# Performance work log

Hardware: AMD Instinct MI355X
Metric: run time of the kernel (lower is better)

The kernel has to match this reference:

```python
import jax, jax.numpy as jnp
import numpy as np

D_MODEL = 128; N_HEADS = 8; N_LEVELS = 1; N_POINTS = 8
MAX_RES = 10.0
B, H_SP, W_SP = 8, 64, 64


def setup_inputs() -> dict:
    key = jax.random.key(0)
    ks = jax.random.split(key, 8)
    s = 0.02
    f32 = jnp.float32
    return {
        "nbr_fea": jax.random.normal(ks[0], (B, D_MODEL, H_SP, W_SP), f32),
        "ext_fea": jax.random.normal(ks[1], (B, D_MODEL, H_SP, W_SP), f32),
        "W_val": jax.random.normal(ks[2], (D_MODEL, D_MODEL), f32) * s,
        "b_val": jnp.zeros((D_MODEL,), f32),
        "W_off": jax.random.normal(ks[3], (D_MODEL, N_HEADS * N_LEVELS * N_POINTS * 2), f32) * s,
        "b_off": jax.random.normal(ks[4], (N_HEADS * N_LEVELS * N_POINTS * 2,), f32) * s,
        "W_attn": jax.random.normal(ks[5], (D_MODEL, N_HEADS * N_LEVELS * N_POINTS), f32) * s,
        "b_attn": jnp.zeros((N_HEADS * N_LEVELS * N_POINTS,), f32),
        "W_out": jax.random.normal(ks[6], (D_MODEL, D_MODEL), f32) * s,
        "b_out": jnp.zeros((D_MODEL,), f32),
    }


def _deform_attn_align(nbr_fea, ext_fea, W_val, b_val, W_off, b_off, W_attn, b_attn, W_out, b_out):
    b, c, h, w = nbr_fea.shape
    L = h * w
    dh = c // N_HEADS
    # flatten b c h w -> b (h w) c
    query = jnp.transpose(ext_fea, (0, 2, 3, 1)).reshape(b, L, c)
    vin = jnp.transpose(nbr_fea, (0, 2, 3, 1)).reshape(b, L, c)

    # value projection (mask is all-False -> no masked fill needed)
    value = (vin @ W_val + b_val).reshape(b, L, N_HEADS, dh)
    vh = jnp.transpose(value, (0, 2, 1, 3))  # [b, H, L, dh]

    # sampling offsets, clamped by max_residue_magnitude * tanh
    off = MAX_RES * jnp.tanh(query @ W_off + b_off)
    off = off.reshape(b, L, N_HEADS, N_POINTS, 2)  # single level
    attn = jax.nn.softmax((query @ W_attn + b_attn).reshape(b, L, N_HEADS, N_POINTS), axis=-1)

    # reference points in [0,1]; valid_ratio == 1 since padding mask is all-False
    yy, xx = jnp.meshgrid(jnp.arange(h, dtype=jnp.float32), jnp.arange(w, dtype=jnp.float32), indexing="ij")
    ref = jnp.stack([(xx.reshape(-1) + 0.5) / w, (yy.reshape(-1) + 0.5) / h], axis=-1)  # [L, 2]
    norm = jnp.array([w, h], jnp.float32)  # offset_normalizer [W, H]
    loc = ref[None, :, None, None, :] + off / norm  # [b, L, H, P, 2]

    # grid_sample(align_corners=False, padding_mode='zeros') pixel coordinates
    px = jnp.transpose(loc[..., 0] * w - 0.5, (0, 2, 1, 3))  # [b, H, L, P]
    py = jnp.transpose(loc[..., 1] * h - 0.5, (0, 2, 1, 3))

    x0 = jnp.floor(px); y0 = jnp.floor(py)
    fx = px - x0; fy = py - y0
    x0i = x0.astype(jnp.int32); y0i = y0.astype(jnp.int32)

    def gather(xi, yi):
        valid = (xi >= 0) & (xi < w) & (yi >= 0) & (yi < h)
        idx = jnp.clip(yi, 0, h - 1) * w + jnp.clip(xi, 0, w - 1)  # [b, H, L, P]
        g = jnp.take_along_axis(vh, idx.reshape(b, N_HEADS, L * N_POINTS)[..., None], axis=2)
        return g.reshape(b, N_HEADS, L, N_POINTS, dh) * valid[..., None]

    samp = (gather(x0i, y0i) * ((1.0 - fx) * (1.0 - fy))[..., None]
            + gather(x0i + 1, y0i) * (fx * (1.0 - fy))[..., None]
            + gather(x0i, y0i + 1) * ((1.0 - fx) * fy)[..., None]
            + gather(x0i + 1, y0i + 1) * (fx * fy)[..., None])  # [b, H, L, P, dh]

    aw = jnp.transpose(attn, (0, 2, 1, 3))  # [b, H, L, P]
    out = jnp.sum(samp * aw[..., None], axis=3)  # [b, H, L, dh]
    out = jnp.transpose(out, (0, 2, 1, 3)).reshape(b, L, c)
    out = out @ W_out + b_out
    return jnp.transpose(out.reshape(b, h, w, c), (0, 3, 1, 2))  # b c h w


def reference(nbr_fea, ext_fea, W_val, b_val, W_off, b_off, W_attn, b_attn, W_out, b_out):
    return _deform_attn_align(nbr_fea, ext_fea, W_val, b_val, W_off, b_off, W_attn, b_attn, W_out, b_out)
```

## Files before the change

### kernel.cpp

```cpp
#include <hip/hip_runtime.h>
#include <cstdint>

#define HB 8
#define CM 128
#define NHEAD 8
#define NPT 8
#define DHD 16
#define HS 64
#define WS 64
#define LTOT 4096
#define NQA 192

typedef float floatx4 __attribute__((ext_vector_type(4)));
typedef short bf16x8 __attribute__((ext_vector_type(8)));

__device__ __forceinline__ unsigned short f2bf_rne(float x) {
  unsigned u = __float_as_uint(x);
  return (unsigned short)((u + 0x7FFFu + ((u >> 16) & 1)) >> 16);
}
__device__ __forceinline__ void split_bf(float x, unsigned short& h, unsigned short& l) {
  unsigned u = __float_as_uint(x);
  h = (unsigned short)(u >> 16);
  float r = x - __uint_as_float(u & 0xFFFF0000u);
  l = (unsigned short)(__float_as_uint(r) >> 16);
}
__device__ __forceinline__ float fast_tanh(float x) {
  float e = __expf(2.0f * x);
  return 1.0f - 2.0f / (e + 1.0f);
}

__global__ __launch_bounds__(256) void prep(const float* __restrict__ Wv,
                                            const float* __restrict__ Wo,
                                            const float* __restrict__ Wa,
                                            const float* __restrict__ Ww,
                                            const float* __restrict__ bo,
                                            const float* __restrict__ ba,
                                            unsigned short* __restrict__ wf_val,
                                            unsigned short* __restrict__ wf_qa,
                                            unsigned short* __restrict__ wf_out,
                                            float* __restrict__ bias_qa) {
  const int gid = blockIdx.x * 256 + threadIdx.x;
  const int k4 = gid / 448;
  const int ng = gid - k4 * 448;

  const float* src;
  unsigned short* dst;
  int Nsrc, Nn, nd, n;
  if (ng < 128) {        src = Wv; dst = wf_val; Nsrc = 128; Nn = 128; n = ng;        nd = n; }
  else if (ng < 256) {   src = Wo; dst = wf_qa;  Nsrc = 128; Nn = 192; n = ng - 128;  nd = n; }
  else if (ng < 320) {   src = Wa; dst = wf_qa;  Nsrc = 64;  Nn = 192; n = ng - 256;  nd = n + 128; }
  else {                 src = Ww; dst = wf_out; Nsrc = 128; Nn = 128; n = ng - 320;  nd = n; }

  ushort4 hi, lo;
  split_bf(src[(k4 * 4 + 0) * Nsrc + n], hi.x, lo.x);
  split_bf(src[(k4 * 4 + 1) * Nsrc + n], hi.y, lo.y);
  split_bf(src[(k4 * 4 + 2) * Nsrc + n], hi.z, lo.z);
  split_bf(src[(k4 * 4 + 3) * Nsrc + n], hi.w, lo.w);
  const int off = (k4 >> 1) * Nn * 8 + nd * 8 + (k4 & 1) * 4;
  *(ushort4*)(dst + off) = hi;
  *(ushort4*)(dst + Nn * 128 + off) = lo;

  if (gid < 128) bias_qa[gid] = bo[gid];
  else if (gid < 192) bias_qa[gid] = ba[gid - 128];
}

template <int N, int OUT_MODE>
__device__ __forceinline__ void gemm_wide(const float* __restrict__ A,
                                          const unsigned short* __restrict__ WF,
                                          const float* __restrict__ bias,
                                          float* __restrict__ out,
                                          int b, int ml0, int t, char* smem) {
  constexpr int NT = N / 32;
  unsigned short* AB = (unsigned short*)smem;

  {
    const float* src = A + (size_t)b * CM * LTOT + ml0;
    const int x = t & 63, kq = t >> 6;
#pragma unroll
    for (int i = 0; i < 8; i++) {
      const int kb = kq * 4 + i * 16;
      ushort4 hi, lo;
      split_bf(src[(size_t)(kb + 0) * LTOT + x], hi.x, lo.x);
      split_bf(src[(size_t)(kb + 1) * LTOT + x], hi.y, lo.y);
      split_bf(src[(size_t)(kb + 2) * LTOT + x], hi.z, lo.z);
      split_bf(src[(size_t)(kb + 3) * LTOT + x], hi.w, lo.w);
      const int off = x * 128 + (((kb >> 3) ^ (x & 15)) << 3) + (kb & 7);
      *(ushort4*)(AB + off) = hi;
      *(ushort4*)(AB + 8192 + off) = lo;
    }
  }
  __syncthreads();

  const int w = t >> 6, lane = t & 63;
  const int wm = (w >> 1) * 32, wn = (w & 1) * (N / 2);
  const int nl = lane & 15, q = lane >> 4;

  floatx4 acc[2][NT];
#pragma unroll
  for (int mt = 0; mt < 2; mt++)
#pragma unroll
    for (int j = 0; j < NT; j++) acc[mt][j] = {0.0f, 0.0f, 0.0f, 0.0f};

#pragma unroll
  for (int K0 = 0; K0 < 4; K0++) {
    bf16x8 ah[2], al[2];
#pragma unroll
    for (int mt = 0; mt < 2; mt++) {
      const int m = wm + mt * 16 + nl;
      const int off = m * 128 + (((K0 * 4 + q) ^ (m & 15)) << 3);
      ah[mt] = *(bf16x8*)(AB + off);
      al[mt] = *(bf16x8*)(AB + 8192 + off);
    }
#pragma unroll
    for (int j = 0; j < NT; j++) {
      const int n = wn + j * 16 + nl;
      const size_t o = (size_t)(K0 * 4 + q) * N * 8 + n * 8;
      const bf16x8 wh = *(const bf16x8*)(WF + o);
      const bf16x8 wl = *(const bf16x8*)(WF + (size_t)N * 128 + o);
#pragma unroll
      for (int mt = 0; mt < 2; mt++) {
        acc[mt][j] = __builtin_amdgcn_mfma_f32_16x16x32_bf16(al[mt], wh, acc[mt][j], 0, 0, 0);
        acc[mt][j] = __builtin_amdgcn_mfma_f32_16x16x32_bf16(ah[mt], wl, acc[mt][j], 0, 0, 0);
        acc[mt][j] = __builtin_amdgcn_mfma_f32_16x16x32_bf16(ah[mt], wh, acc[mt][j], 0, 0, 0);
      }
    }
  }

#pragma unroll
  for (int j = 0; j < NT; j++) {
    const int gc = wn + j * 16 + nl;
    const float bv = bias[gc];
#pragma unroll
    for (int mt = 0; mt < 2; mt++)
#pragma unroll
      for (int r = 0; r < 4; r++) {
        const int m = ml0 + wm + mt * 16 + q * 4 + r;
        const float v = acc[mt][j][r] + bv;
        if (OUT_MODE == 0)
          out[(((size_t)b * NHEAD + (gc >> 4)) * LTOT + m) * DHD + (gc & 15)] = v;
        else
          out[((size_t)b * LTOT + m) * NQA + gc] = v;
      }
  }
}

__global__ __launch_bounds__(256, 4) void gemm_vq(const float* __restrict__ nbr,
                                                  const float* __restrict__ ext,
                                                  const unsigned short* __restrict__ wf_val,
                                                  const unsigned short* __restrict__ wf_qa,
                                                  const float* __restrict__ b_val,
                                                  const float* __restrict__ bias_qa,
                                                  float* __restrict__ value,
                                                  float* __restrict__ qa) {
  __shared__ char smem[32768];
  if (blockIdx.y == 0)
    gemm_wide<128, 0>(nbr, wf_val, b_val, value, blockIdx.z, blockIdx.x * 64, threadIdx.x, smem);
  else
    gemm_wide<192, 1>(ext, wf_qa, bias_qa, qa, blockIdx.z, blockIdx.x * 64, threadIdx.x, smem);
}

__global__ __launch_bounds__(512, 2) void samp_out(const float* __restrict__ value,
                                                   const float* __restrict__ qa,
                                                   const unsigned short* __restrict__ wf_out,
                                                   const float* __restrict__ b_out,
                                                   float* __restrict__ out) {
  __shared__ char smem[33280];
  unsigned short* FR = (unsigned short*)smem;
  const int t = threadIdx.x;
  const int b = blockIdx.y;
  const int ml0 = blockIdx.x * 64;
  const int d4 = t & 3;
  const int u = t >> 2;

#pragma unroll
  for (int ps = 0; ps < 4; ps++) {
    const int idx = ps * 128 + u;
    const int ll = idx >> 3;
    const int h = idx & 7;
    const int l = ml0 + ll;
    const size_t bl = (size_t)b * LTOT + l;
    const float* qrow = qa + bl * NQA;

    float4 of[4];
#pragma unroll
    for (int j = 0; j < 4; j++) of[j] = *(const float4*)(qrow + h * 16 + j * 4);
    const float4 lga = *(const float4*)(qrow + 128 + h * 8);
    const float4 lgb = *(const float4*)(qrow + 128 + h * 8 + 4);
    float lg[8] = {lga.x, lga.y, lga.z, lga.w, lgb.x, lgb.y, lgb.z, lgb.w};

    float m = lg[0];
#pragma unroll
    for (int p = 1; p < 8; p++) m = fmaxf(m, lg[p]);
    float e[8], s = 0.0f;
#pragma unroll
    for (int p = 0; p < 8; p++) { e[p] = __expf(lg[p] - m); s += e[p]; }
    const float inv = 1.0f / s;

    const float xf = (float)(l & (WS - 1));
    const float yf = (float)(l >> 6);
    const float* vb = value + ((size_t)b * NHEAD + h) * (LTOT * DHD) + d4 * 4;

    float4 o = {0.0f, 0.0f, 0.0f, 0.0f};
#pragma unroll
    for (int p = 0; p < 8; p++) {
      const float ox = (p & 1) ? of[p >> 1].z : of[p >> 1].x;
      const float oy = (p & 1) ? of[p >> 1].w : of[p >> 1].y;
      const float aw = e[p] * inv;
      const float px = xf + 10.0f * fast_tanh(ox);
      const float py = yf + 10.0f * fast_tanh(oy);
      const float x0f = floorf(px), y0f = floorf(py);
      const float fx = px - x0f, fy = py - y0f;
      const int ix = (int)x0f, iy = (int)y0f;
#pragma unroll
      for (int c = 0; c < 4; c++) {
        const int cdx = c & 1, cdy = c >> 1;
        const int jx = ix + cdx, jy = iy + cdy;
        const float wx = cdx ? fx : 1.0f - fx;
        const float wy = cdy ? fy : 1.0f - fy;
        const bool valid = ((unsigned)jx < WS) & ((unsigned)jy < HS);
        const float wc = valid ? aw * wx * wy : 0.0f;
        const int cx = min(max(jx, 0), WS - 1);
        const int cy = min(max(jy, 0), HS - 1);
        const float4 v = *(const float4*)(vb + (size_t)((cy << 6) + cx) * DHD);
        o.x += wc * v.x;
        o.y += wc * v.y;
        o.z += wc * v.z;
        o.w += wc * v.w;
      }
    }

    const int off = ll * 128 + (((h * 2 + (d4 >> 1)) ^ (ll & 15)) << 3) + (d4 & 1) * 4;
    ushort4 st = {f2bf_rne(o.x), f2bf_rne(o.y), f2bf_rne(o.z), f2bf_rne(o.w)};
    *(ushort4*)(FR + off) = st;
  }
  __syncthreads();

  const int w = t >> 6, lane = t & 63;
  const int nl = lane & 15, q = lane >> 4;
  const int wm = (w >> 1) * 16;
  const int wn = (w & 1) * 64;

  floatx4 acc[4];
#pragma unroll
  for (int j = 0; j < 4; j++) acc[j] = {0.0f, 0.0f, 0.0f, 0.0f};

#pragma unroll
  for (int K0 = 0; K0 < 4; K0++) {
    const int m = wm + nl;
    const int off = m * 128 + (((K0 * 4 + q) ^ (m & 15)) << 3);
    const bf16x8 ah = *(bf16x8*)(FR + off);
#pragma unroll
    for (int j = 0; j < 4; j++) {
      const int n = wn + j * 16 + nl;
      const size_t o = (size_t)(K0 * 4 + q) * CM * 8 + n * 8;
      const bf16x8 wh = *(const bf16x8*)(wf_out + o);
      const bf16x8 wl = *(const bf16x8*)(wf_out + (size_t)CM * 128 + o);
      acc[j] = __builtin_amdgcn_mfma_f32_16x16x32_bf16(ah, wl, acc[j], 0, 0, 0);
      acc[j] = __builtin_amdgcn_mfma_f32_16x16x32_bf16(ah, wh, acc[j], 0, 0, 0);
    }
  }

  __syncthreads();
  float* LF = (float*)smem;
#pragma unroll
  for (int j = 0; j < 4; j++) {
    const int n = wn + j * 16 + nl;
#pragma unroll
    for (int r = 0; r < 4; r++) LF[n * 65 + wm + q * 4 + r] = acc[j][r];
  }
  __syncthreads();

#pragma unroll
  for (int i = 0; i < 16; i++) {
    const int idx = t + i * 512;
    const int n = idx >> 6, m = idx & 63;
    out[((size_t)b * CM + n) * LTOT + ml0 + m] = LF[n * 65 + m] + b_out[n];
  }
}

extern "C" void kernel_launch(void* const* d_in, const int* in_sizes, int n_in,
                              void* d_out, int out_size, void* d_ws, size_t ws_size,
                              hipStream_t stream) {
  const float* nbr    = (const float*)d_in[0];
  const float* ext    = (const float*)d_in[1];
  const float* W_val  = (const float*)d_in[2];
  const float* b_val  = (const float*)d_in[3];
  const float* W_off  = (const float*)d_in[4];
  const float* b_off  = (const float*)d_in[5];
  const float* W_attn = (const float*)d_in[6];
  const float* b_attn = (const float*)d_in[7];
  const float* W_out  = (const float*)d_in[8];
  const float* b_out  = (const float*)d_in[9];
  float* out = (float*)d_out;

  float* value = (float*)d_ws;
  float* qa    = value + (size_t)HB * NHEAD * LTOT * DHD;
  unsigned short* wf_val = (unsigned short*)(qa + (size_t)HB * LTOT * NQA);
  unsigned short* wf_qa  = wf_val + 128 * 128 * 2;
  unsigned short* wf_out = wf_qa + 192 * 128 * 2;
  float* bias_qa = (float*)(wf_out + 128 * 128 * 2);

  prep<<<56, 256, 0, stream>>>(W_val, W_off, W_attn, W_out, b_off, b_attn,
                               wf_val, wf_qa, wf_out, bias_qa);
  gemm_vq<<<dim3(64, 2, HB), 256, 0, stream>>>(nbr, ext, wf_val, wf_qa, b_val, bias_qa, value, qa);
  samp_out<<<dim3(64, HB), 512, 0, stream>>>(value, qa, wf_out, b_out, out);
}
```

Before: 158.1 us.

## Store value projection in bf16, precompute sample coords in LDS, interleave batch blocks

```diff
diff --git a/kernel.cpp b/kernel.cpp
--- a/kernel.cpp
+++ b/kernel.cpp
@@ -68,7 +68,7 @@
 __device__ __forceinline__ void gemm_wide(const float* __restrict__ A,
                                           const unsigned short* __restrict__ WF,
                                           const float* __restrict__ bias,
-                                          float* __restrict__ out,
+                                          void* __restrict__ outv,
                                           int b, int ml0, int t, char* smem) {
   constexpr int NT = N / 32;
   unsigned short* AB = (unsigned short*)smem;
@@ -137,9 +137,10 @@
         const int m = ml0 + wm + mt * 16 + q * 4 + r;
         const float v = acc[mt][j][r] + bv;
         if (OUT_MODE == 0)
-          out[(((size_t)b * NHEAD + (gc >> 4)) * LTOT + m) * DHD + (gc & 15)] = v;
+          ((unsigned short*)outv)[(((size_t)b * NHEAD + (gc >> 4)) * LTOT + m) * DHD + (gc & 15)] =
+              f2bf_rne(v);
         else
-          out[((size_t)b * LTOT + m) * NQA + gc] = v;
+          ((float*)outv)[((size_t)b * LTOT + m) * NQA + gc] = v;
       }
   }
 }
@@ -150,7 +151,7 @@
                                                   const unsigned short* __restrict__ wf_qa,
                                                   const float* __restrict__ b_val,
                                                   const float* __restrict__ bias_qa,
-                                                  float* __restrict__ value,
+                                                  unsigned short* __restrict__ value,
                                                   float* __restrict__ qa) {
   __shared__ char smem[32768];
   if (blockIdx.y == 0)
@@ -159,35 +160,30 @@
     gemm_wide<192, 1>(ext, wf_qa, bias_qa, qa, blockIdx.z, blockIdx.x * 64, threadIdx.x, smem);
 }
 
-__global__ __launch_bounds__(512, 2) void samp_out(const float* __restrict__ value,
+__global__ __launch_bounds__(512, 2) void samp_out(const unsigned short* __restrict__ value,
                                                    const float* __restrict__ qa,
                                                    const unsigned short* __restrict__ wf_out,
                                                    const float* __restrict__ b_out,
                                                    float* __restrict__ out) {
-  __shared__ char smem[33280];
-  unsigned short* FR = (unsigned short*)smem;
+  __shared__ char smem[65536];
+  float2* WXY = (float2*)smem;
+  float* WA = (float*)(smem + 32768);
+  unsigned short* FR = (unsigned short*)(smem + 49152);
   const int t = threadIdx.x;
-  const int b = blockIdx.y;
-  const int ml0 = blockIdx.x * 64;
-  const int d4 = t & 3;
-  const int u = t >> 2;
-
-#pragma unroll
-  for (int ps = 0; ps < 4; ps++) {
-    const int idx = ps * 128 + u;
-    const int ll = idx >> 3;
-    const int h = idx & 7;
+  const int b = blockIdx.x & 7;
+  const int tile = blockIdx.x >> 3;
+  const int ml0 = tile * 64;
+
+  {
+    const int ll = t >> 3, h = t & 7;
     const int l = ml0 + ll;
-    const size_t bl = (size_t)b * LTOT + l;
-    const float* qrow = qa + bl * NQA;
-
+    const float* qrow = qa + ((size_t)b * LTOT + l) * NQA;
     float4 of[4];
 #pragma unroll
     for (int j = 0; j < 4; j++) of[j] = *(const float4*)(qrow + h * 16 + j * 4);
     const float4 lga = *(const float4*)(qrow + 128 + h * 8);
     const float4 lgb = *(const float4*)(qrow + 128 + h * 8 + 4);
-    float lg[8] = {lga.x, lga.y, lga.z, lga.w, lgb.x, lgb.y, lgb.z, lgb.w};
-
+    const float lg[8] = {lga.x, lga.y, lga.z, lga.w, lgb.x, lgb.y, lgb.z, lgb.w};
     float m = lg[0];
 #pragma unroll
     for (int p = 1; p < 8; p++) m = fmaxf(m, lg[p]);
@@ -195,21 +191,34 @@
 #pragma unroll
     for (int p = 0; p < 8; p++) { e[p] = __expf(lg[p] - m); s += e[p]; }
     const float inv = 1.0f / s;
-
     const float xf = (float)(l & (WS - 1));
     const float yf = (float)(l >> 6);
-    const float* vb = value + ((size_t)b * NHEAD + h) * (LTOT * DHD) + d4 * 4;
-
-    float4 o = {0.0f, 0.0f, 0.0f, 0.0f};
 #pragma unroll
     for (int p = 0; p < 8; p++) {
       const float ox = (p & 1) ? of[p >> 1].z : of[p >> 1].x;
       const float oy = (p & 1) ? of[p >> 1].w : of[p >> 1].y;
-      const float aw = e[p] * inv;
-      const float px = xf + 10.0f * fast_tanh(ox);
-      const float py = yf + 10.0f * fast_tanh(oy);
-      const float x0f = floorf(px), y0f = floorf(py);
-      const float fx = px - x0f, fy = py - y0f;
+      WXY[p * 512 + t] = {xf + 10.0f * fast_tanh(ox), yf + 10.0f * fast_tanh(oy)};
+      WA[p * 512 + t] = e[p] * inv;
+    }
+  }
+  __syncthreads();
+
+  const int d4 = t & 3;
+  const int u = t >> 2;
+#pragma unroll
+  for (int ps = 0; ps < 4; ps++) {
+    const int uu = ps * 128 + u;
+    const int ll = uu >> 3;
+    const int h = uu & 7;
+    const unsigned short* vbb = value + ((size_t)(b * NHEAD + h) * LTOT) * DHD + d4 * 4;
+
+    float4 o = {0.0f, 0.0f, 0.0f, 0.0f};
+#pragma unroll
+    for (int p = 0; p < 8; p++) {
+      const float2 pxy = WXY[p * 512 + uu];
+      const float aw = WA[p * 512 + uu];
+      const float x0f = floorf(pxy.x), y0f = floorf(pxy.y);
+      const float fx = pxy.x - x0f, fy = pxy.y - y0f;
       const int ix = (int)x0f, iy = (int)y0f;
 #pragma unroll
       for (int c = 0; c < 4; c++) {
@@ -221,11 +230,11 @@
         const float wc = valid ? aw * wx * wy : 0.0f;
         const int cx = min(max(jx, 0), WS - 1);
         const int cy = min(max(jy, 0), HS - 1);
-        const float4 v = *(const float4*)(vb + (size_t)((cy << 6) + cx) * DHD);
-        o.x += wc * v.x;
-        o.y += wc * v.y;
-        o.z += wc * v.z;
-        o.w += wc * v.w;
+        const uint2 rw = *(const uint2*)(vbb + (size_t)((cy << 6) + cx) * DHD);
+        o.x += wc * __uint_as_float(rw.x << 16);
+        o.y += wc * __uint_as_float(rw.x & 0xFFFF0000u);
+        o.z += wc * __uint_as_float(rw.y << 16);
+        o.w += wc * __uint_as_float(rw.y & 0xFFFF0000u);
       }
     }
 
@@ -293,8 +302,8 @@
   const float* b_out  = (const float*)d_in[9];
   float* out = (float*)d_out;
 
-  float* value = (float*)d_ws;
-  float* qa    = value + (size_t)HB * NHEAD * LTOT * DHD;
+  unsigned short* value = (unsigned short*)d_ws;
+  float* qa = (float*)(value + (size_t)HB * NHEAD * LTOT * DHD);
   unsigned short* wf_val = (unsigned short*)(qa + (size_t)HB * LTOT * NQA);
   unsigned short* wf_qa  = wf_val + 128 * 128 * 2;
   unsigned short* wf_out = wf_qa + 192 * 128 * 2;
@@ -303,5 +312,5 @@
   prep<<<56, 256, 0, stream>>>(W_val, W_off, W_attn, W_out, b_off, b_attn,
                                wf_val, wf_qa, wf_out, bias_qa);
   gemm_vq<<<dim3(64, 2, HB), 256, 0, stream>>>(nbr, ext, wf_val, wf_qa, b_val, bias_qa, value, qa);
-  samp_out<<<dim3(64, HB), 512, 0, stream>>>(value, qa, wf_out, b_out, out);
-}
+  samp_out<<<dim3(512), 512, 0, stream>>>(value, qa, wf_out, b_out, out);
+}
```

After: 136.1 us. -13.9%, faster.
